# Optimization experiments

Measured on AMD Instinct MI355X. Metric: run time of the kernel, lower is better.

## Reference

```python
import jax, jax.numpy as jnp
import numpy as np

B, L, D1, D2, N = 4, 2048, 1024, 1024, 4096

def setup_inputs() -> dict:
    key = jax.random.key(0)
    k1, k2, k3 = jax.random.split(key, 3)
    inputs = jax.random.normal(k1, (B, L, D1), dtype=jnp.float32)
    key_param_tokens = jax.random.normal(k2, (N, D1), dtype=jnp.float32) * 0.02
    value_param_tokens = jax.random.normal(k3, (N, D2), dtype=jnp.float32) * 0.02
    return {"inputs": inputs, "key_param_tokens": key_param_tokens, "value_param_tokens": value_param_tokens}

def reference(inputs, key_param_tokens, value_param_tokens):
    # scores: [B, L, N] = query @ key^T (scale_factor = 1, no mask, dropout_p = 0)
    attn_weight = jnp.einsum('bld,nd->bln', inputs, key_param_tokens)
    n = attn_weight.shape[-1]
    # 'l2_norm_gelu': L2-normalize over the param-token axis, rescale by sqrt(n), then exact GELU
    l2 = jnp.sqrt(jnp.sum(attn_weight * attn_weight, axis=-1, keepdims=True))
    normed = attn_weight / l2 * jnp.sqrt(jnp.asarray(n, attn_weight.dtype))
    attn_weight = jax.nn.gelu(normed, approximate=False)
    # output: [B, L, D2]
    return jnp.einsum('bln,nd->bld', attn_weight, value_param_tokens)
```

## Files before the change

kernel.cpp:

```cpp
#include <hip/hip_runtime.h>
#include <hip/hip_bf16.h>
#include <math.h>
#include <stdint.h>

typedef __attribute__((ext_vector_type(8))) short short8;
typedef __attribute__((ext_vector_type(4))) float f32x4;

__device__ inline short f2bf(float x) {
  union { float f; uint32_t u; } c; c.f = x;
  uint32_t r = (c.u + 0x7FFFu + ((c.u >> 16) & 1u)) >> 16;
  return (short)(uint16_t)r;
}
__device__ inline float bf2f(short s) {
  union { uint32_t u; float f; } c; c.u = ((uint32_t)(uint16_t)s) << 16;
  return c.f;
}

__device__ inline void gload16(const short* src, const char* ldsdst) {
  __builtin_amdgcn_global_load_lds(
      (const __attribute__((address_space(1))) void*)src,
      (__attribute__((address_space(3))) void*)ldsdst, 16, 0, 0);
}

#define BAR __builtin_amdgcn_s_barrier()
#define LGKM0                                          \
  do {                                                 \
    asm volatile("s_waitcnt lgkmcnt(0)" ::: "memory"); \
    __builtin_amdgcn_sched_barrier(0);                 \
  } while (0)
#define VMC(n) asm volatile("s_waitcnt vmcnt(" #n ")" ::: "memory")

__global__ void f32_to_bf16_kernel(const float* __restrict__ in,
                                   short* __restrict__ out, int n8) {
  int i = blockIdx.x * blockDim.x + threadIdx.x;
  if (i >= n8) return;
  const float4* p = (const float4*)(in + (size_t)i * 8);
  float4 a = p[0], b = p[1];
  short8 o;
  o[0] = f2bf(a.x); o[1] = f2bf(a.y); o[2] = f2bf(a.z); o[3] = f2bf(a.w);
  o[4] = f2bf(b.x); o[5] = f2bf(b.y); o[6] = f2bf(b.z); o[7] = f2bf(b.w);
  *(short8*)(out + (size_t)i * 8) = o;
}

__global__ void transpose_bf16_kernel(const float* __restrict__ V,
                                      short* __restrict__ Vt,
                                      int rows, int cols) {
  __shared__ float tile[64][65];
  int n0 = blockIdx.x * 64;
  int d0 = blockIdx.y * 64;
  int t = threadIdx.x;
#pragma unroll
  for (int r = 0; r < 16; ++r) {
    int idx = t + 256 * r;
    int rr = idx >> 6, cc = idx & 63;
    tile[rr][cc] = V[(size_t)(n0 + rr) * cols + d0 + cc];
  }
  __syncthreads();
#pragma unroll
  for (int r = 0; r < 16; ++r) {
    int idx = t + 256 * r;
    int dd = idx >> 6, nn = idx & 63;
    Vt[(size_t)(d0 + dd) * rows + n0 + nn] = f2bf(tile[nn][dd]);
  }
}

__global__ __launch_bounds__(512, 2) void gemm1_kernel(
    const short* __restrict__ A, const short* __restrict__ B,
    short* __restrict__ S, float* __restrict__ rowss) {
  constexpr int K = 1024, N = 4096, NT = K / 64;
  __shared__ char lds[2 * 65536];
  const int t = threadIdx.x, lane = t & 63, w = t >> 6;
  const int wm = w >> 2, wn = w & 3;
  const int idx = lane & 15, g = lane >> 4;
  const int bid = blockIdx.x;
  const int id2 = (bid & 7) * 64 + (bid >> 3);
  const int row0 = (id2 >> 4) * 256, col0 = (id2 & 15) * 256;

  const int srow = t >> 3;
  const int ksl = (t & 7) ^ (srow & 7);
  const short* gA = A + (size_t)(row0 + srow) * K + ksl * 8;
  const short* gB = B + (size_t)(col0 + srow) * K + ksl * 8;

  auto stageA = [&](int buf, int frow, int kt) {
#pragma unroll
    for (int r = 0; r < 2; ++r)
      gload16(gA + (size_t)(frow + r * 64) * K + kt,
              &lds[buf * 65536 + (frow + r * 64) * 128 + t * 16]);
  };
  auto stageB = [&](int buf, int frow, int kt) {
#pragma unroll
    for (int r = 0; r < 2; ++r)
      gload16(gB + (size_t)(frow + r * 64) * K + kt,
              &lds[buf * 65536 + 32768 + (frow + r * 64) * 128 + t * 16]);
  };

  const int xv = (idx & 7) << 4;
  short8 a[4][2], b[2][2][2];
  auto lda = [&](int buf, int mh) {
#pragma unroll
    for (int f = 0; f < 4; ++f)
#pragma unroll
      for (int ks = 0; ks < 2; ++ks) {
        int row = mh * 128 + wm * 64 + f * 16 + idx;
        int byte = row * 128 + ((ks * 64 + g * 16) ^ xv);
        a[f][ks] = *(const short8*)&lds[buf * 65536 + byte];
      }
  };
  auto ldb = [&](int buf, int nh) {
#pragma unroll
    for (int nf = 0; nf < 2; ++nf)
#pragma unroll
      for (int ks = 0; ks < 2; ++ks) {
        int col = nh * 128 + wn * 32 + nf * 16 + idx;
        int byte = col * 128 + ((ks * 64 + g * 16) ^ xv);
        b[nh][nf][ks] = *(const short8*)&lds[buf * 65536 + 32768 + byte];
      }
  };

  f32x4 acc[8][4] = {};
  auto MF = [&](int mh, int nh) {
    __builtin_amdgcn_s_setprio(1);
#pragma unroll
    for (int ks = 0; ks < 2; ++ks)
#pragma unroll
      for (int f = 0; f < 4; ++f)
#pragma unroll
        for (int n = 0; n < 2; ++n)
          acc[mh * 4 + f][nh * 2 + n] = __builtin_amdgcn_mfma_f32_16x16x32_bf16(
              a[f][ks], b[nh][n][ks], acc[mh * 4 + f][nh * 2 + n], 0, 0, 0);
    __builtin_amdgcn_s_setprio(0);
    __builtin_amdgcn_sched_barrier(0);
  };

  stageA(0, 0, 0);
  stageB(0, 0, 0);
  stageB(0, 128, 0);
  stageA(0, 128, 0);
  VMC(4);
  BAR;

  for (int tb = 0; tb < NT; tb += 2) {
#pragma unroll
    for (int u = 0; u < 2; ++u) {
      const int T = tb + u, buf = u, nbuf = u ^ 1;
      const int kt1 = (T + 1) * 64;
      const bool more = (T + 1 < NT);
      lda(buf, 0); ldb(buf, 0);
      if (more) stageA(nbuf, 0, kt1);
      BAR; LGKM0; MF(0, 0);
      if (more) { VMC(4); } else { VMC(2); }
      BAR;
      ldb(buf, 1);
      if (more) stageB(nbuf, 0, kt1);
      BAR; LGKM0; MF(0, 1);
      if (more) { VMC(4); } else { VMC(0); }
      BAR;
      lda(buf, 1);
      if (more) stageB(nbuf, 128, kt1);
      BAR; LGKM0; MF(1, 1);
      BAR;
      if (more) stageA(nbuf, 128, kt1);
      BAR; MF(1, 0);
      if (more) VMC(4);
      BAR;
    }
  }

#pragma unroll
  for (int mf = 0; mf < 8; ++mf) {
#pragma unroll
    for (int j = 0; j < 4; ++j) {
      const int row = row0 + wm * 64 + (mf & 3) * 16 + (mf >> 2) * 128 + g * 4 + j;
      float ss = 0.f;
#pragma unroll
      for (int nf = 0; nf < 4; ++nf) {
        const float v = acc[mf][nf][j];
        ss += v * v;
        const int col = col0 + wn * 32 + (nf & 1) * 16 + (nf >> 1) * 128 + idx;
        S[(size_t)row * N + col] = f2bf(v);
      }
      ss += __shfl_xor(ss, 1);
      ss += __shfl_xor(ss, 2);
      ss += __shfl_xor(ss, 4);
      ss += __shfl_xor(ss, 8);
      if (idx == 0) atomicAdd(&rowss[row], ss);
    }
  }
}

__global__ __launch_bounds__(512, 2) void gemm2_kernel(
    const short* __restrict__ A, const short* __restrict__ B,
    float* __restrict__ C) {
  constexpr int K = 4096, N = 1024, NT = K / 64;
  __shared__ char lds[2 * 49152];
  const int t = threadIdx.x, lane = t & 63, w = t >> 6;
  const int wm = w >> 1, wn = w & 1;
  const int idx = lane & 15, g = lane >> 4;
  const int bid = blockIdx.x;
  const int id2 = (bid & 7) * 32 + (bid >> 3);
  const int row0 = (id2 >> 3) * 256, col0 = (id2 & 7) * 128;

  const int srow = t >> 3;
  const int ksl = (t & 7) ^ (srow & 7);
  const short* gA = A + (size_t)(row0 + srow) * K + ksl * 8;
  const short* gB = B + (size_t)(col0 + srow) * K + ksl * 8;

  auto stageAr = [&](int buf, int fr, int kt) {
    gload16(gA + (size_t)(fr)*K + kt, &lds[buf * 49152 + fr * 128 + t * 16]);
  };
  auto stageB = [&](int buf, int kt) {
#pragma unroll
    for (int r = 0; r < 2; ++r)
      gload16(gB + (size_t)(r * 64) * K + kt,
              &lds[buf * 49152 + 32768 + r * 8192 + t * 16]);
  };

  const int xv = (idx & 7) << 4;
  short8 a[2][2], b[4][2];
  auto lda = [&](int buf, int mh) {
#pragma unroll
    for (int f = 0; f < 2; ++f)
#pragma unroll
      for (int ks = 0; ks < 2; ++ks) {
        int row = mh * 128 + wm * 32 + f * 16 + idx;
        int byte = row * 128 + ((ks * 64 + g * 16) ^ xv);
        a[f][ks] = *(const short8*)&lds[buf * 49152 + byte];
      }
  };
  auto ldb = [&](int buf) {
#pragma unroll
    for (int nf = 0; nf < 4; ++nf)
#pragma unroll
      for (int ks = 0; ks < 2; ++ks) {
        int col = wn * 64 + nf * 16 + idx;
        int byte = col * 128 + ((ks * 64 + g * 16) ^ xv);
        b[nf][ks] = *(const short8*)&lds[buf * 49152 + 32768 + byte];
      }
  };

  f32x4 acc[4][4] = {};
  auto MF = [&](int mh) {
    __builtin_amdgcn_s_setprio(1);
#pragma unroll
    for (int ks = 0; ks < 2; ++ks)
#pragma unroll
      for (int f = 0; f < 2; ++f)
#pragma unroll
        for (int nf = 0; nf < 4; ++nf)
          acc[mh * 2 + f][nf] = __builtin_amdgcn_mfma_f32_16x16x32_bf16(
              a[f][ks], b[nf][ks], acc[mh * 2 + f][nf], 0, 0, 0);
    __builtin_amdgcn_s_setprio(0);
    __builtin_amdgcn_sched_barrier(0);
  };

  stageB(0, 0);
  stageAr(0, 0, 0);
  stageAr(0, 64, 0);
  stageAr(0, 128, 0);
  stageAr(0, 192, 0);
  VMC(2);
  BAR;

  for (int tb = 0; tb < NT; tb += 2) {
#pragma unroll
    for (int u = 0; u < 2; ++u) {
      const int T = tb + u, buf = u, nbuf = u ^ 1;
      const int kt1 = (T + 1) * 64;
      const bool more = (T + 1 < NT);
      ldb(buf); lda(buf, 0);
      if (more) { stageB(nbuf, kt1); stageAr(nbuf, 0, kt1); }
      BAR; LGKM0; MF(0);
      if (more) { VMC(3); } else { VMC(0); }
      BAR;
      lda(buf, 1);
      if (more) { stageAr(nbuf, 64, kt1); stageAr(nbuf, 128, kt1); stageAr(nbuf, 192, kt1); }
      BAR; LGKM0; MF(1);
      if (more) VMC(2);
      BAR;
    }
  }

#pragma unroll
  for (int mf = 0; mf < 4; ++mf)
#pragma unroll
    for (int j = 0; j < 4; ++j) {
      const int row = row0 + wm * 32 + (mf & 1) * 16 + (mf >> 1) * 128 + g * 4 + j;
#pragma unroll
      for (int nf = 0; nf < 4; ++nf)
        C[(size_t)row * N + col0 + wn * 64 + nf * 16 + idx] = acc[mf][nf][j];
    }
}

__global__ void norm_gelu_kernel(short* __restrict__ S,
                                 const float* __restrict__ rowss, int total8) {
  int i = blockIdx.x * blockDim.x + threadIdx.x;
  if (i >= total8) return;
  size_t base = (size_t)i * 8;
  int row = (int)(base >> 12);
  float scale = 64.0f * rsqrtf(rowss[row]);
  short8 v = *(short8*)(S + base);
  short8 o;
#pragma unroll
  for (int k = 0; k < 8; ++k) {
    float x = bf2f(v[k]) * scale;
    float gl = 0.5f * x * (1.0f + erff(x * 0.70710678118654752f));
    o[k] = f2bf(gl);
  }
  *(short8*)(S + base) = o;
}

extern "C" void kernel_launch(void* const* d_in, const int* in_sizes, int n_in,
                              void* d_out, int out_size, void* d_ws,
                              size_t ws_size, hipStream_t stream) {
  const float* X = (const float*)d_in[0];
  const float* Kp = (const float*)d_in[1];
  const float* Vp = (const float*)d_in[2];
  float* out = (float*)d_out;

  const int M = 8192, D1 = 1024, Nn = 4096, D2 = 1024;

  char* ws = (char*)d_ws;
  short* Xb = (short*)ws; ws += (size_t)M * D1 * 2;
  short* Kb = (short*)ws; ws += (size_t)Nn * D1 * 2;
  short* Vt = (short*)ws; ws += (size_t)D2 * Nn * 2;
  short* S  = (short*)ws; ws += (size_t)M * Nn * 2;
  float* rowss = (float*)ws;
  (void)ws_size;

  hipMemsetAsync(rowss, 0, M * sizeof(float), stream);
  f32_to_bf16_kernel<<<(M * D1 / 8 + 255) / 256, 256, 0, stream>>>(X, Xb, M * D1 / 8);
  f32_to_bf16_kernel<<<(Nn * D1 / 8 + 255) / 256, 256, 0, stream>>>(Kp, Kb, Nn * D1 / 8);
  transpose_bf16_kernel<<<dim3(Nn / 64, D2 / 64), 256, 0, stream>>>(Vp, Vt, Nn, D2);

  gemm1_kernel<<<512, 512, 0, stream>>>(Xb, Kb, S, rowss);
  norm_gelu_kernel<<<(M * Nn / 8 + 255) / 256, 256, 0, stream>>>(S, rowss, M * Nn / 8);
  gemm2_kernel<<<256, 512, 0, stream>>>(S, Vt, out);
}
```

Measured before the change: 203.7 us.

## Remove redundant barriers and lgkm waits in both GEMM main loops

```diff
diff --git a/kernel.cpp b/kernel.cpp
--- a/kernel.cpp
+++ b/kernel.cpp
@@ -23,11 +23,6 @@
 }
 
 #define BAR __builtin_amdgcn_s_barrier()
-#define LGKM0                                          \
-  do {                                                 \
-    asm volatile("s_waitcnt lgkmcnt(0)" ::: "memory"); \
-    __builtin_amdgcn_sched_barrier(0);                 \
-  } while (0)
 #define VMC(n) asm volatile("s_waitcnt vmcnt(" #n ")" ::: "memory")
 
 __global__ void f32_to_bf16_kernel(const float* __restrict__ in,
@@ -129,14 +124,13 @@
           acc[mh * 4 + f][nh * 2 + n] = __builtin_amdgcn_mfma_f32_16x16x32_bf16(
               a[f][ks], b[nh][n][ks], acc[mh * 4 + f][nh * 2 + n], 0, 0, 0);
     __builtin_amdgcn_s_setprio(0);
-    __builtin_amdgcn_sched_barrier(0);
   };
 
   stageA(0, 0, 0);
   stageB(0, 0, 0);
   stageB(0, 128, 0);
   stageA(0, 128, 0);
-  VMC(4);
+  VMC(2);
   BAR;
 
   for (int tb = 0; tb < NT; tb += 2) {
@@ -147,22 +141,21 @@
       const bool more = (T + 1 < NT);
       lda(buf, 0); ldb(buf, 0);
       if (more) stageA(nbuf, 0, kt1);
-      BAR; LGKM0; MF(0, 0);
-      if (more) { VMC(4); } else { VMC(2); }
-      BAR;
+      MF(0, 0);
       ldb(buf, 1);
       if (more) stageB(nbuf, 0, kt1);
-      BAR; LGKM0; MF(0, 1);
+      MF(0, 1);
       if (more) { VMC(4); } else { VMC(0); }
       BAR;
       lda(buf, 1);
       if (more) stageB(nbuf, 128, kt1);
-      BAR; LGKM0; MF(1, 1);
-      BAR;
+      MF(1, 1);
       if (more) stageA(nbuf, 128, kt1);
-      BAR; MF(1, 0);
-      if (more) VMC(4);
-      BAR;
+      MF(1, 0);
+      if (more) {
+        VMC(2);
+        BAR;
+      }
     }
   }
 
@@ -250,7 +243,6 @@
           acc[mh * 2 + f][nf] = __builtin_amdgcn_mfma_f32_16x16x32_bf16(
               a[f][ks], b[nf][ks], acc[mh * 2 + f][nf], 0, 0, 0);
     __builtin_amdgcn_s_setprio(0);
-    __builtin_amdgcn_sched_barrier(0);
   };
 
   stageB(0, 0);
@@ -268,15 +260,17 @@
       const int kt1 = (T + 1) * 64;
       const bool more = (T + 1 < NT);
       ldb(buf); lda(buf, 0);
-      if (more) { stageB(nbuf, kt1); stageAr(nbuf, 0, kt1); }
-      BAR; LGKM0; MF(0);
-      if (more) { VMC(3); } else { VMC(0); }
+      if (more) { stageB(nbuf, kt1); stageAr(nbuf, 0, kt1); stageAr(nbuf, 64, kt1); }
+      MF(0);
+      if (more) { VMC(4); } else { VMC(0); }
       BAR;
       lda(buf, 1);
-      if (more) { stageAr(nbuf, 64, kt1); stageAr(nbuf, 128, kt1); stageAr(nbuf, 192, kt1); }
-      BAR; LGKM0; MF(1);
-      if (more) VMC(2);
-      BAR;
+      if (more) { stageAr(nbuf, 128, kt1); stageAr(nbuf, 192, kt1); }
+      MF(1);
+      if (more) {
+        VMC(2);
+        BAR;
+      }
     }
   }
 
```

Measured after the change: 194.4 us. 1.05x faster.
